# Kernel optimization log

Hardware: AMD Instinct MI355X
Metric: run time of the kernel (lower is better)

## Reference

```python
import jax, jax.numpy as jnp
import numpy as np

B, L, N_SAMPLES = 16, 512, 512
N_REF = 1000


def _interp_row(xs, ys, q):
    # Linear interpolation with linear extrapolation at both ends,
    # matching torchinterp1d: ind = clamp(searchsorted(x, q) - 1, 0, n-2).
    n = xs.shape[0]
    i = jnp.clip(jnp.searchsorted(xs, q, side='left') - 1, 0, n - 2)
    x0 = xs[i]
    y0 = ys[i]
    slope = (ys[i + 1] - y0) / (xs[i + 1] - x0)
    return y0 + slope * (q - x0)


def interp1d(x, y, xq):
    # x, y: [b, l, n] (x sorted along last dim); xq: [b, l, m]
    b, l, n = x.shape
    m = xq.shape[-1]
    out = jax.vmap(_interp_row)(x.reshape(-1, n), y.reshape(-1, n), xq.reshape(-1, m))
    return out.reshape(b, l, m)


def emb(samples, ref):
    # samples: [b, l, n] circular samples in [0,1); ref: [N]
    b, l, n = samples.shape
    N = ref.shape[0]
    dt = samples.dtype

    xs = jnp.sort(samples, axis=-1)                                  # [b,l,n]
    ys = jnp.broadcast_to(jnp.arange(1, n + 1, dtype=dt) / n, (b, l, n))

    xnew = jnp.broadcast_to(jnp.linspace(-1.0, 2.0, 3 * N, dtype=dt), (b, l, 3 * N))
    int_x = jnp.floor(xnew)
    rest_x = xnew - int_x
    # circular ECDF extended to [-1, 2)
    ecdf_vals = int_x + interp1d(xs, ys, rest_x)                     # [b,l,3N]

    alpha = jnp.mean(samples, axis=-1, keepdims=True) - 0.5          # [b,l,1]
    x = jnp.broadcast_to(ref.astype(dt), (b, l, N))
    # inverse CDF (quantile) evaluated at x - alpha, minus identity map
    return interp1d(ecdf_vals, xnew, x - alpha) - x                  # [b,l,N]


def setup_inputs() -> dict:
    key = jax.random.key(0)
    k1, k2 = jax.random.split(key)
    x1 = jax.random.uniform(k1, (B, L, N_SAMPLES), dtype=jnp.float32)
    x2 = jax.random.uniform(k2, (B, L, N_SAMPLES), dtype=jnp.float32)
    ref = jnp.arange(N_REF, dtype=jnp.float32) / N_REF  # linspace(0,1,1001)[:-1]
    return {"x1": x1, "x2": x2, "ref": ref}


def reference(x1, x2, ref):
    e1 = emb(x1, ref)
    e2 = emb(x2, ref)
    d = jnp.abs(e2 - e1)
    circ = jnp.minimum(d, 1.0 - d)                                   # circular distance
    return jnp.sqrt(jnp.sum(circ * circ, axis=-1)).mean(-1)          # [b]
```

## Files before the change

kernel.cpp:

```cpp
#include <hip/hip_runtime.h>
#include <math.h>

#define NB 16
#define NL 512
#define NS 512
#define NE 3000
#define NR 1000
#define NROWS (NB * NL)
#define NBIN 512

__device__ __forceinline__ float fast_rcp(float x) { return __builtin_amdgcn_rcpf(x); }

__global__ __launch_bounds__(256) void lcot_row_kernel(
    const float* __restrict__ x1, const float* __restrict__ x2,
    const float* __restrict__ ref, float* __restrict__ row_out)
{
    __shared__ float    s_sorted[NS];
    __shared__ unsigned s_hist[NBIN];
    __shared__ unsigned s_prefix[NBIN + 1];
    __shared__ float    s_ecdf[NE];
    __shared__ float    s_alpA[4], s_alpB[4];
    __shared__ float    s_devf[4];
    __shared__ unsigned s_wredu[4];

    const int tid  = threadIdx.x;
    const int lane = tid & 63;
    const int wave = tid >> 6;
    const int row  = blockIdx.x;
    const float inv_n   = 1.0f / 512.0f;
    const float step    = (float)(3.0 / 2999.0);
    const float invstep = 2999.0f / 3.0f;

    const int j0 = tid * 4;
    float rj0 = 0.f, rj1 = 0.f, rj2 = 0.f, rj3 = 0.f;
    if (j0 < NR) {
        float4 r4 = ((const float4*)ref)[tid];
        rj0 = r4.x; rj1 = r4.y; rj2 = r4.z; rj3 = r4.w;
    }
    float e1r0 = 0.f, e1r1 = 0.f, e1r2 = 0.f, e1r3 = 0.f;

    const float* srcA = x1 + (size_t)row * NS;
    const float* srcB = x2 + (size_t)row * NS;
    float a0 = srcA[tid], a1 = srcA[tid + 256];
    float c0 = srcB[tid], c1 = srcB[tid + 256];

    float acc = 0.0f;

    for (int inp = 0; inp < 2; ++inp) {
        float v0 = (inp == 0) ? a0 : c0;
        float v1 = (inp == 0) ? a1 : c1;

        if (inp == 0) {
            s_hist[tid] = 0u;
            s_hist[tid + 256] = 0u;
            float sA = a0 + a1, sB = c0 + c1;
            #pragma unroll
            for (int o = 32; o > 0; o >>= 1) {
                sA += __shfl_down(sA, o, 64);
                sB += __shfl_down(sB, o, 64);
            }
            if (lane == 0) { s_alpA[wave] = sA; s_alpB[wave] = sB; }
            __syncthreads();
        }

        int b0 = min((int)(v0 * 512.0f), NBIN - 1);
        int b1 = min((int)(v1 * 512.0f), NBIN - 1);
        atomicAdd(&s_hist[b0], 1u);
        atomicAdd(&s_hist[b1], 1u);
        __syncthreads();

        const float* alp = (inp == 0) ? s_alpA : s_alpB;
        float alpha = (alp[0] + alp[1] + alp[2] + alp[3]) * inv_n - 0.5f;

        unsigned h0 = s_hist[2 * tid];
        unsigned h1 = s_hist[2 * tid + 1];
        unsigned ls = h0 + h1;
        unsigned sc0 = ls;
        #pragma unroll
        for (int o = 1; o < 64; o <<= 1) {
            unsigned t2 = __shfl_up(sc0, o, 64);
            if (lane >= o) sc0 += t2;
        }
        if (lane == 63) s_wredu[wave] = sc0;
        __syncthreads();
        unsigned wbase0 = 0;
        for (int w = 0; w < 4; ++w) if (w < wave) wbase0 += s_wredu[w];
        unsigned base = wbase0 + sc0 - ls;
        s_prefix[2 * tid]     = base;
        s_prefix[2 * tid + 1] = base + h0;
        s_hist[2 * tid]       = base;
        s_hist[2 * tid + 1]   = base + h0;
        if (tid == 255) s_prefix[NBIN] = (unsigned)NS;
        __syncthreads();

        unsigned p0 = atomicAdd(&s_hist[b0], 1u);
        s_sorted[p0] = v0;
        unsigned p1 = atomicAdd(&s_hist[b1], 1u);
        s_sorted[p1] = v1;
        float dv = fmaxf(fabsf((float)(p0 + 1) * inv_n - v0),
                         fabsf((float)(p1 + 1) * inv_n - v1));
        #pragma unroll
        for (int o = 32; o > 0; o >>= 1) dv = fmaxf(dv, __shfl_down(dv, o, 64));
        if (lane == 0) s_devf[wave] = dv;
        __syncthreads();

        for (int bb = tid; bb < NBIN; bb += 256) {
            int beg = (int)s_prefix[bb];
            int end = (int)s_prefix[bb + 1];
            for (int i2 = beg + 1; i2 < end; ++i2) {
                float key = s_sorted[i2];
                int jj = i2 - 1;
                while (jj >= beg && s_sorted[jj] > key) { s_sorted[jj + 1] = s_sorted[jj]; --jj; }
                s_sorted[jj + 1] = key;
            }
        }
        __syncthreads();

        float Dm = fmaxf(fmaxf(s_devf[0], s_devf[1]), fmaxf(s_devf[2], s_devf[3]));
        {
            float sa0 = s_sorted[0], sa1 = s_sorted[1];
            float sbA = s_sorted[510], sbB = s_sorted[511];
            float sl0 = inv_n * fast_rcp(sa1 - sa0);
            float slR = inv_n * fast_rcp(sbB - sbA);
            float lext = fabsf(inv_n - sl0 * sa0);
            float rext = fabsf(511.0f * inv_n + slR * (1.0f - sbA) - 1.0f);
            Dm = fmaxf(Dm, fmaxf(lext, rext));
        }
        float D = Dm + 0.0249f;

        float qlo = 0.0f - alpha;
        float qhi = 0.999f - alpha;
        int kmin = max(0,  (int)((qlo + 1.0f - D) * invstep) - 2);
        int kmax = min(NE, (int)((qhi + 1.0f + D) * invstep) + 3);

        {
            int W  = kmax - kmin;
            int k0 = kmin + ((tid * W) >> 8);
            int k1 = kmin + (((tid + 1) * W) >> 8);
            if (k0 < k1) {
                int sgA = k0 / 1000;
                int sgB = (k1 - 1) / 1000;
                for (int sg = sgA; sg <= sgB; ++sg) {
                    int ka = max(k0, sg * 1000);
                    int kb = min(k1, sg * 1000 + 1000);
                    float fm = (float)(sg - 1);
                    float xn0 = -1.0f + (float)ka * step;
                    float r0  = xn0 - fm;
                    int bq  = min((int)(r0 * 512.0f), NBIN - 1);
                    int pos = (int)s_prefix[bq];
                    int be  = (int)s_prefix[bq + 1];
                    while (pos < be && s_sorted[pos] < r0) ++pos;
                    float snext = (pos < NS) ? s_sorted[pos] : 2.0f;
                    int i = min(max(pos - 1, 0), NS - 2);
                    int ci = i;
                    float cx0 = s_sorted[i];
                    float cy0 = (float)(i + 1) * inv_n;
                    float csl = inv_n * fast_rcp(s_sorted[i + 1] - cx0);
                    for (int k = ka; k < kb; ++k) {
                        float xn = -1.0f + (float)k * step;
                        float r  = xn - fm;
                        while (pos < NS && snext < r) {
                            ++pos;
                            snext = (pos < NS) ? s_sorted[pos] : 2.0f;
                        }
                        i = min(max(pos - 1, 0), NS - 2);
                        if (i != ci) {
                            ci = i;
                            cx0 = s_sorted[i];
                            cy0 = (float)(i + 1) * inv_n;
                            csl = inv_n * fast_rcp(s_sorted[i + 1] - cx0);
                        }
                        s_ecdf[k] = fm + (cy0 + csl * (r - cx0));
                    }
                }
            }
        }
        if (inp == 0) { s_hist[tid] = 0u; s_hist[tid + 256] = 0u; }
        __syncthreads();

        if (j0 < NR) {
            float q = rj0 - alpha;
            int lo = max(kmin, (int)((q - D + 1.0f) * invstep) - 2);
            int hi = min(kmax, (int)((q + D + 1.0f) * invstep) + 3);
            while (lo < hi) {
                int mid = (lo + hi) >> 1;
                if (s_ecdf[mid] < q) lo = mid + 1; else hi = mid;
            }
            int pos2 = lo;
            #pragma unroll
            for (int jj = 0; jj < 4; ++jj) {
                float rj = (jj == 0) ? rj0 : (jj == 1) ? rj1 : (jj == 2) ? rj2 : rj3;
                q = rj - alpha;
                if (jj > 0) while (pos2 < NE && s_ecdf[pos2] < q) ++pos2;
                int i = min(max(pos2 - 1, 0), NE - 2);
                float e0 = s_ecdf[i];
                float slope = step * fast_rcp(s_ecdf[i + 1] - e0);
                float xn0 = -1.0f + (float)i * step;
                float res = xn0 + slope * (q - e0);
                float embv = res - rj;
                if (inp == 0) {
                    if (jj == 0) e1r0 = embv;
                    else if (jj == 1) e1r1 = embv;
                    else if (jj == 2) e1r2 = embv;
                    else e1r3 = embv;
                } else {
                    float ev = (jj == 0) ? e1r0 : (jj == 1) ? e1r1 : (jj == 2) ? e1r2 : e1r3;
                    float d = fabsf(embv - ev);
                    float c = fminf(d, 1.0f - d);
                    acc = fmaf(c, c, acc);
                }
            }
        }
    }

    #pragma unroll
    for (int o = 32; o > 0; o >>= 1) acc += __shfl_down(acc, o, 64);
    if (lane == 0) s_devf[wave] = acc;
    __syncthreads();
    if (tid == 0) row_out[row] = sqrtf(s_devf[0] + s_devf[1] + s_devf[2] + s_devf[3]);
}

__global__ __launch_bounds__(256) void lcot_reduce_kernel(
    const float* __restrict__ row_vals, float* __restrict__ out)
{
    __shared__ float s_red[256];
    const int b = blockIdx.x;
    const int tid = threadIdx.x;
    float v = row_vals[b * NL + tid] + row_vals[b * NL + tid + 256];
    s_red[tid] = v;
    __syncthreads();
    for (int off = 128; off > 0; off >>= 1) {
        if (tid < off) s_red[tid] += s_red[tid + off];
        __syncthreads();
    }
    if (tid == 0) out[b] = s_red[0] * (1.0f / (float)NL);
}

extern "C" void kernel_launch(void* const* d_in, const int* in_sizes, int n_in,
                              void* d_out, int out_size, void* d_ws, size_t ws_size,
                              hipStream_t stream) {
    const float* x1  = (const float*)d_in[0];
    const float* x2  = (const float*)d_in[1];
    const float* ref = (const float*)d_in[2];
    float* out = (float*)d_out;
    float* row_vals = (float*)d_ws;

    lcot_row_kernel<<<NROWS, 256, 0, stream>>>(x1, x2, ref, row_vals);
    lcot_reduce_kernel<<<NB, 256, 0, stream>>>(row_vals, out);
}
```

Measured before the change: 103.2 us.

## Scatter quantile cell indices during ECDF build to replace per-query binary search

While building the ECDF window, each thread now records, for every reference point whose target value falls between consecutive grid values, the grid cell index in a shared table. The query phase then reads that cell directly instead of binary-searching the ECDF, keeping the binary search only for points near the non-monotone seams at the grid boundaries. The ECDF buffer is also shrunk to a capped window offset by kmin. This adds per-cell scatter work, an extra sync and bridge evaluation, and a risk of mismatched indices near the boundaries.

```diff
diff --git a/kernel.cpp b/kernel.cpp
--- a/kernel.cpp
+++ b/kernel.cpp
@@ -8,8 +8,29 @@
 #define NR 1000
 #define NROWS (NB * NL)
 #define NBIN 512
+#define WCAP 2048
 
 __device__ __forceinline__ float fast_rcp(float x) { return __builtin_amdgcn_rcpf(x); }
+
+__device__ __forceinline__ float evalF(const float* __restrict__ xs,
+                                       const unsigned* __restrict__ prefix,
+                                       int k)
+{
+    const float step  = (float)(3.0 / 2999.0);
+    const float inv_n = 1.0f / 512.0f;
+    float xn = -1.0f + (float)k * step;
+    float fm = floorf(xn);
+    float r  = xn - fm;
+    int b  = min((int)(r * 512.0f), NBIN - 1);
+    int p  = (int)prefix[b];
+    int pe = (int)prefix[b + 1];
+    while (p < pe && xs[p] < r) ++p;
+    int i = min(max(p - 1, 0), NS - 2);
+    float x0 = xs[i];
+    float y0 = (float)(i + 1) * inv_n;
+    float slope = inv_n * fast_rcp(xs[i + 1] - x0);
+    return fm + (y0 + slope * (r - x0));
+}
 
 __global__ __launch_bounds__(256) void lcot_row_kernel(
     const float* __restrict__ x1, const float* __restrict__ x2,
@@ -18,7 +39,9 @@
     __shared__ float    s_sorted[NS];
     __shared__ unsigned s_hist[NBIN];
     __shared__ unsigned s_prefix[NBIN + 1];
-    __shared__ float    s_ecdf[NE];
+    __shared__ float    s_ecdfw[WCAP];
+    __shared__ unsigned short s_cellof[NR];
+    __shared__ float    s_bridgef[4];
     __shared__ float    s_alpA[4], s_alpB[4];
     __shared__ float    s_devf[4];
     __shared__ unsigned s_wredu[4];
@@ -116,6 +139,12 @@
         }
         __syncthreads();
 
+        if (tid < 4) {
+            int kb = ((tid >> 1) ? 1999 : 999) + (tid & 1);
+            s_bridgef[tid] = evalF(s_sorted, s_prefix, kb);
+        }
+        __syncthreads();
+
         float Dm = fmaxf(fmaxf(s_devf[0], s_devf[1]), fmaxf(s_devf[2], s_devf[3]));
         {
             float sa0 = s_sorted[0], sa1 = s_sorted[1];
@@ -132,12 +161,22 @@
         float qhi = 0.999f - alpha;
         int kmin = max(0,  (int)((qlo + 1.0f - D) * invstep) - 2);
         int kmax = min(NE, (int)((qhi + 1.0f + D) * invstep) + 3);
+        kmax = min(kmax, kmin + WCAP);
+
+        float t0a = s_bridgef[0], t0b = s_bridgef[1];
+        float t1a = s_bridgef[2], t1b = s_bridgef[3];
+        int jA0 = max(0,      (int)floorf((t0b + alpha) * 1000.0f) + 1);
+        int jA1 = min(NR - 1, (int)floorf((t0a + alpha) * 1000.0f));
+        int jB0 = max(0,      (int)floorf((t1b + alpha) * 1000.0f) + 1);
+        int jB1 = min(NR - 1, (int)floorf((t1a + alpha) * 1000.0f));
 
         {
             int W  = kmax - kmin;
             int k0 = kmin + ((tid * W) >> 8);
             int k1 = kmin + (((tid + 1) * W) >> 8);
             if (k0 < k1) {
+                int  jcur = 0;
+                bool first = true;
                 int sgA = k0 / 1000;
                 int sgB = (k1 - 1) / 1000;
                 for (int sg = sgA; sg <= sgB; ++sg) {
@@ -145,32 +184,52 @@
                     int kb = min(k1, sg * 1000 + 1000);
                     float fm = (float)(sg - 1);
                     float xn0 = -1.0f + (float)ka * step;
-                    float r0  = xn0 - fm;
-                    int bq  = min((int)(r0 * 512.0f), NBIN - 1);
+                    float r   = xn0 - fm;
+                    int bq  = min((int)(r * 512.0f), NBIN - 1);
                     int pos = (int)s_prefix[bq];
                     int be  = (int)s_prefix[bq + 1];
-                    while (pos < be && s_sorted[pos] < r0) ++pos;
+                    while (pos < be && s_sorted[pos] < r) ++pos;
                     float snext = (pos < NS) ? s_sorted[pos] : 2.0f;
                     int i = min(max(pos - 1, 0), NS - 2);
                     int ci = i;
                     float cx0 = s_sorted[i];
                     float cy0 = (float)(i + 1) * inv_n;
                     float csl = inv_n * fast_rcp(s_sorted[i + 1] - cx0);
+                    float Fk = fm + (cy0 + csl * (r - cx0));
+                    if (first) {
+                        jcur = min(1000, max(0, (int)floorf((Fk + alpha) * 1000.0f) + 1));
+                        first = false;
+                    }
                     for (int k = ka; k < kb; ++k) {
-                        float xn = -1.0f + (float)k * step;
-                        float r  = xn - fm;
-                        while (pos < NS && snext < r) {
-                            ++pos;
-                            snext = (pos < NS) ? s_sorted[pos] : 2.0f;
+                        s_ecdfw[k - kmin] = Fk;
+                        float Fn;
+                        if (k + 1 < kb) {
+                            float xn2 = -1.0f + (float)(k + 1) * step;
+                            float r2  = xn2 - fm;
+                            while (pos < NS && snext < r2) {
+                                ++pos;
+                                snext = (pos < NS) ? s_sorted[pos] : 2.0f;
+                            }
+                            i = min(max(pos - 1, 0), NS - 2);
+                            if (i != ci) {
+                                ci = i;
+                                cx0 = s_sorted[i];
+                                cy0 = (float)(i + 1) * inv_n;
+                                csl = inv_n * fast_rcp(s_sorted[i + 1] - cx0);
+                            }
+                            Fn = fm + (cy0 + csl * (r2 - cx0));
+                        } else {
+                            Fn = evalF(s_sorted, s_prefix, k + 1);
                         }
-                        i = min(max(pos - 1, 0), NS - 2);
-                        if (i != ci) {
-                            ci = i;
-                            cx0 = s_sorted[i];
-                            cy0 = (float)(i + 1) * inv_n;
-                            csl = inv_n * fast_rcp(s_sorted[i + 1] - cx0);
+                        if (k < kmax - 1) {
+                            int jnext = min(1000, (int)floorf((Fn + alpha) * 1000.0f) + 1);
+                            for (int j = jcur; j < jnext; ++j) {
+                                bool amb_ = (j >= jA0 && j <= jA1) || (j >= jB0 && j <= jB1);
+                                if (!amb_) s_cellof[j] = (unsigned short)(k - kmin);
+                            }
+                            if (jnext > jcur) jcur = jnext;
                         }
-                        s_ecdf[k] = fm + (cy0 + csl * (r - cx0));
+                        Fk = Fn;
                     }
                 }
             }
@@ -179,25 +238,29 @@
         __syncthreads();
 
         if (j0 < NR) {
-            float q = rj0 - alpha;
-            int lo = max(kmin, (int)((q - D + 1.0f) * invstep) - 2);
-            int hi = min(kmax, (int)((q + D + 1.0f) * invstep) + 3);
-            while (lo < hi) {
-                int mid = (lo + hi) >> 1;
-                if (s_ecdf[mid] < q) lo = mid + 1; else hi = mid;
-            }
-            int pos2 = lo;
             #pragma unroll
             for (int jj = 0; jj < 4; ++jj) {
+                int   j  = j0 + jj;
                 float rj = (jj == 0) ? rj0 : (jj == 1) ? rj1 : (jj == 2) ? rj2 : rj3;
-                q = rj - alpha;
-                if (jj > 0) while (pos2 < NE && s_ecdf[pos2] < q) ++pos2;
-                int i = min(max(pos2 - 1, 0), NE - 2);
-                float e0 = s_ecdf[i];
-                float slope = step * fast_rcp(s_ecdf[i + 1] - e0);
-                float xn0 = -1.0f + (float)i * step;
-                float res = xn0 + slope * (q - e0);
-                float embv = res - rj;
+                float q  = rj - alpha;
+                bool amb_ = (j >= jA0 && j <= jA1) || (j >= jB0 && j <= jB1);
+                int kq;
+                if (amb_) {
+                    int lo = max(kmin, (int)((q - D + 1.0f) * invstep) - 2);
+                    int hi = min(kmax, (int)((q + D + 1.0f) * invstep) + 3);
+                    while (lo < hi) {
+                        int mid = (lo + hi) >> 1;
+                        if (s_ecdfw[mid - kmin] < q) lo = mid + 1; else hi = mid;
+                    }
+                    kq = min(max(lo - 1, kmin), kmax - 2);
+                } else {
+                    kq = kmin + (int)s_cellof[j];
+                }
+                float e0  = s_ecdfw[kq - kmin];
+                float e1c = s_ecdfw[kq - kmin + 1];
+                float slope = step * fast_rcp(e1c - e0);
+                float xn0 = -1.0f + (float)kq * step;
+                float embv = xn0 + slope * (q - e0) - rj;
                 if (inp == 0) {
                     if (jj == 0) e1r0 = embv;
                     else if (jj == 1) e1r1 = embv;
```

Result: slower. 194.8 us (+88.8%).
